# Kernel tuning notes

Measured on AMD Instinct MI355X. Metric: run time of the kernel, lower is better.

Reference implementation:

```python
import jax, jax.numpy as jnp
import numpy as np

B, S, D, H, DK, DV = 4, 4096, 512, 8, 64, 64
BUCKET = 64
NB = S // BUCKET  # number of hash buckets = 64


def layernorm(x, g, b, eps=1e-5):
    m = x.mean(-1, keepdims=True)
    v = ((x - m) ** 2).mean(-1, keepdims=True)
    return (x - m) * jax.lax.rsqrt(v + eps) * g + b


def lsh_attention(x_q, x_kv, Wq, Wk, Wv, Wo, g, b, rot, bucket_size):
    # x_q, x_kv: [B, S, D]; rot: [H, dk, NB//2] random LSH rotations
    Bq, Sq, _ = x_q.shape
    Hh, dk, _ = rot.shape
    q = jnp.einsum('bsd,dhk->bhsk', x_q, Wq)
    k = jnp.einsum('bsd,dhk->bhsk', x_kv, Wk)
    v = jnp.einsum('bsd,dhk->bhsk', x_kv, Wv)
    dv = v.shape[-1]

    def hash_buckets(t):
        r = jnp.einsum('bhsk,hkr->bhsr', t, rot)
        return jnp.argmax(jnp.concatenate([r, -r], axis=-1), axis=-1)  # [B,H,S]

    bq = hash_buckets(q)
    bk = hash_buckets(k)
    pos = jnp.arange(Sq)
    # stable sort by bucket (position breaks ties)
    perm_q = jnp.argsort(bq * Sq + pos, axis=-1)  # [B,H,S]
    perm_k = jnp.argsort(bk * Sq + pos, axis=-1)
    take = lambda t, p: jnp.take_along_axis(t, p[..., None], axis=2)
    nc = Sq // bucket_size
    cq = take(q, perm_q).reshape(Bq, Hh, nc, bucket_size, dk)
    ck = take(k, perm_k).reshape(Bq, Hh, nc, bucket_size, dk)
    cv = take(v, perm_k).reshape(Bq, Hh, nc, bucket_size, dv)
    bq_c = jnp.take_along_axis(bq, perm_q, axis=-1).reshape(Bq, Hh, nc, bucket_size)
    bk_c = jnp.take_along_axis(bk, perm_k, axis=-1).reshape(Bq, Hh, nc, bucket_size)
    # each query chunk attends to its own key chunk plus the previous one
    ckx = jnp.concatenate([jnp.roll(ck, 1, axis=2), ck], axis=3)
    cvx = jnp.concatenate([jnp.roll(cv, 1, axis=2), cv], axis=3)
    bkx = jnp.concatenate([jnp.roll(bk_c, 1, axis=2), bk_c], axis=3)
    scores = jnp.einsum('bhcid,bhcjd->bhcij', cq, ckx) * (dk ** -0.5)
    scores = jnp.where(bq_c[..., :, None] == bkx[..., None, :], scores, -1e9)
    attn = jax.nn.softmax(scores, axis=-1)
    o = jnp.einsum('bhcij,bhcjd->bhcid', attn, cvx).reshape(Bq, Hh, Sq, dv)
    o = take(o, jnp.argsort(perm_q, axis=-1))  # unsort
    o = o.transpose(0, 2, 1, 3).reshape(Bq, Sq, Hh * dv)
    return layernorm(x_q + o @ Wo, g, b)


def feed_forward(x, W1, b1, W2, b2, g, b):
    h = jax.nn.relu(x @ W1 + b1)
    return layernorm(x + h @ W2 + b2, g, b)


def setup_inputs() -> dict:
    key = jax.random.key(0)
    ks = jax.random.split(key, 16)
    f = jax.random.normal
    d = {
        'decoder_input': f(ks[0], (B, S, D), jnp.float32),
        'encoder_output': f(ks[1], (B, S, D), jnp.float32),
    }
    s = D ** -0.5
    for i, pfx in ((2, 'sa'), (7, 'ca')):
        d[pfx + '_Wq'] = f(ks[i], (D, H, DK)) * s
        d[pfx + '_Wk'] = f(ks[i + 1], (D, H, DK)) * s
        d[pfx + '_Wv'] = f(ks[i + 2], (D, H, DV)) * s
        d[pfx + '_Wo'] = f(ks[i + 3], (H * DV, D)) * s
        d[pfx + '_g'] = jnp.ones((D,), jnp.float32)
        d[pfx + '_b'] = jnp.zeros((D,), jnp.float32)
        d[pfx + '_rot'] = f(ks[i + 4], (H, DK, NB // 2))
    d['ff_W1'] = f(ks[12], (D, 4 * D)) * s
    d['ff_b1'] = jnp.zeros((4 * D,), jnp.float32)
    d['ff_W2'] = f(ks[13], (4 * D, D)) * ((4 * D) ** -0.5)
    d['ff_b2'] = jnp.zeros((D,), jnp.float32)
    d['ff_g'] = jnp.ones((D,), jnp.float32)
    d['ff_b'] = jnp.zeros((D,), jnp.float32)
    d['bucket_size'] = BUCKET
    return d


def reference(decoder_input, encoder_output, sa_Wq, sa_Wk, sa_Wv, sa_Wo, sa_g, sa_b, sa_rot, ca_Wq, ca_Wk, ca_Wv, ca_Wo, ca_g, ca_b, ca_rot, ff_W1, ff_b1, ff_W2, ff_b2, ff_g, ff_b, bucket_size):
    x = lsh_attention(decoder_input, decoder_input, sa_Wq, sa_Wk, sa_Wv, sa_Wo, sa_g, sa_b, sa_rot, bucket_size)
    x = lsh_attention(x, encoder_output, ca_Wq, ca_Wk, ca_Wv, ca_Wo, ca_g, ca_b, ca_rot, bucket_size)
    return feed_forward(x, ff_W1, ff_b1, ff_W2, ff_b2, ff_g, ff_b)
```

## Files before the change

### kernel.cpp

```cpp
#include <hip/hip_runtime.h>
#include <hip/hip_bf16.h>
#include <math.h>

typedef __hip_bfloat16 bf16;

#define B_ 4
#define S_ 4096
#define D_ 512
#define H_ 8
#define NC_ 64
#define M_ (B_*S_)
#define BH_ (B_*H_)

typedef __attribute__((ext_vector_type(8))) short bfrag;
typedef __attribute__((ext_vector_type(4))) float facc;

static __device__ __forceinline__ float tof(float x){ return x; }
static __device__ __forceinline__ float tof(bf16 x){ return __bfloat162float(x); }

static __device__ __forceinline__ float4 ld4g(const float* p) {
    return *reinterpret_cast<const float4*>(p);
}
static __device__ __forceinline__ float4 ld4g(const bf16* p) {
    short4 s = *reinterpret_cast<const short4*>(p);
    float4 r;
    r.x = __bfloat162float(*reinterpret_cast<const bf16*>(&s.x));
    r.y = __bfloat162float(*reinterpret_cast<const bf16*>(&s.y));
    r.z = __bfloat162float(*reinterpret_cast<const bf16*>(&s.z));
    r.w = __bfloat162float(*reinterpret_cast<const bf16*>(&s.w));
    return r;
}
static __device__ __forceinline__ void st4(float* p, float4 v) {
    *reinterpret_cast<float4*>(p) = v;
}
static __device__ __forceinline__ void st4(bf16* p, float4 v) {
    bf16 b0 = __float2bfloat16(v.x), b1 = __float2bfloat16(v.y);
    bf16 b2 = __float2bfloat16(v.z), b3 = __float2bfloat16(v.w);
    short4 s;
    s.x = *reinterpret_cast<short*>(&b0);
    s.y = *reinterpret_cast<short*>(&b1);
    s.z = *reinterpret_cast<short*>(&b2);
    s.w = *reinterpret_cast<short*>(&b3);
    *reinterpret_cast<short4*>(p) = s;
}

#define GLL(gp, lp) __builtin_amdgcn_global_load_lds( \
    (const __attribute__((address_space(1))) void*)(gp), \
    (__attribute__((address_space(3))) void*)(lp), 16, 0, 0)

template<int OUTMODE, int RES>
__global__ __launch_bounds__(256) void gemm_k(
    const float* __restrict__ A, const float* __restrict__ Bw,
    const float* __restrict__ res, float* __restrict__ out, int N, int K)
{
    const int BK = 32;
    __shared__ float At[32][132];
    __shared__ float Bs[32 * 128];

    int tid = threadIdx.x;
    int wave = tid >> 6;
    int nbx = N >> 7;
    int bx = blockIdx.x % nbx;
    int by = blockIdx.x / nbx;
    int row0 = by << 7;
    int col0 = bx << 7;
    int ty = tid >> 4;
    int tx = tid & 15;

    float acc[8][8];
    #pragma unroll
    for (int i = 0; i < 8; i++)
        #pragma unroll
        for (int j = 0; j < 8; j++) acc[i][j] = 0.f;

    for (int k0 = 0; k0 < K; k0 += BK) {
        #pragma unroll
        for (int c = 0; c < 4; c++) {
            int e = c * 256 + tid;
            GLL(Bw + (size_t)(k0 + (e >> 5)) * N + col0 + ((e & 31) << 2),
                &Bs[c * 1024 + (wave << 8)]);
        }
        #pragma unroll
        for (int c = 0; c < 4; c++) {
            int e = c * 256 + tid;
            int r = e >> 3, k4 = (e & 7) << 2;
            float4 t4 = ld4g(A + (size_t)(row0 + r) * K + k0 + k4);
            At[k4 + 0][r] = t4.x;
            At[k4 + 1][r] = t4.y;
            At[k4 + 2][r] = t4.z;
            At[k4 + 3][r] = t4.w;
        }
        __syncthreads();
        #pragma unroll
        for (int kk = 0; kk < BK; kk++) {
            float4 a0 = *reinterpret_cast<const float4*>(&At[kk][ty * 8]);
            float4 a1 = *reinterpret_cast<const float4*>(&At[kk][ty * 8 + 4]);
            float4 b0 = *reinterpret_cast<const float4*>(&Bs[kk * 128 + tx * 4]);
            float4 b1 = *reinterpret_cast<const float4*>(&Bs[kk * 128 + 64 + tx * 4]);
            float a[8] = {a0.x, a0.y, a0.z, a0.w, a1.x, a1.y, a1.z, a1.w};
            float bb[8] = {b0.x, b0.y, b0.z, b0.w, b1.x, b1.y, b1.z, b1.w};
            #pragma unroll
            for (int i = 0; i < 8; i++)
                #pragma unroll
                for (int j = 0; j < 8; j++) acc[i][j] += a[i] * bb[j];
        }
        __syncthreads();
    }

    #pragma unroll
    for (int i = 0; i < 8; i++) {
        int r = row0 + ty * 8 + i;
        #pragma unroll
        for (int j = 0; j < 8; j++) {
            int c = col0 + ((j >> 2) << 6) + tx * 4 + (j & 3);
            float v = acc[i][j];
            if (RES == 1) v += res[(size_t)r * N + c];
            if (OUTMODE == 0) {
                out[(size_t)r * N + c] = v;
            } else {
                int b = r >> 12, s = r & (S_ - 1);
                int h = c >> 6, kk2 = c & 63;
                out[((size_t)(b * H_ + h) * S_ + s) * 64 + kk2] = v;
            }
        }
    }
}

template<int OUTMODE, int RES, bool BIAS, bool RELU>
__global__ __launch_bounds__(256) void mgemm_k(
    const short* __restrict__ A, const short* __restrict__ Bt,
    const float* __restrict__ bias, const float* __restrict__ res,
    void* __restrict__ out, int N, int K)
{
    __shared__ short As[128 * 32];
    __shared__ short Bs[128 * 32];

    int tid = threadIdx.x;
    int wave = tid >> 6, lane = tid & 63;
    int nbx = N >> 7;
    int bx = blockIdx.x % nbx, by = blockIdx.x / nbx;
    int row0 = by << 7, col0 = bx << 7;
    int wr = wave >> 1, wc = wave & 1;
    int fr = lane & 15, fq = lane >> 4;

    facc acc[4][4];
    facc zero = {0.f, 0.f, 0.f, 0.f};
    #pragma unroll
    for (int m = 0; m < 4; m++)
        #pragma unroll
        for (int n = 0; n < 4; n++) acc[m][n] = zero;

    const short* gA = A + (size_t)(row0 + (wave << 5) + (lane >> 2)) * K + ((lane & 3) << 3);
    const short* gB = Bt + (size_t)(col0 + (wave << 5) + (lane >> 2)) * K + ((lane & 3) << 3);

    for (int k0 = 0; k0 < K; k0 += 32) {
        GLL(gA + k0,                 &As[wave << 10]);
        GLL(gA + k0 + (size_t)16 * K, &As[(wave << 10) + 512]);
        GLL(gB + k0,                 &Bs[wave << 10]);
        GLL(gB + k0 + (size_t)16 * K, &Bs[(wave << 10) + 512]);
        __syncthreads();

        bfrag av[4], bv[4];
        #pragma unroll
        for (int m = 0; m < 4; m++)
            av[m] = *reinterpret_cast<const bfrag*>(&As[(((wr << 6) + (m << 4) + fr) << 5) + (fq << 3)]);
        #pragma unroll
        for (int n = 0; n < 4; n++)
            bv[n] = *reinterpret_cast<const bfrag*>(&Bs[(((wc << 6) + (n << 4) + fr) << 5) + (fq << 3)]);
        #pragma unroll
        for (int m = 0; m < 4; m++)
            #pragma unroll
            for (int n = 0; n < 4; n++)
                acc[m][n] = __builtin_amdgcn_mfma_f32_16x16x32_bf16(av[m], bv[n], acc[m][n], 0, 0, 0);
        __syncthreads();
    }

    #pragma unroll
    for (int m = 0; m < 4; m++) {
        #pragma unroll
        for (int n = 0; n < 4; n++) {
            #pragma unroll
            for (int r = 0; r < 4; r++) {
                int row = row0 + (wr << 6) + (m << 4) + (fq << 2) + r;
                int col = col0 + (wc << 6) + (n << 4) + fr;
                float v = acc[m][n][r];
                if (BIAS) v += bias[col];
                if (RELU) v = fmaxf(v, 0.f);
                if (RES == 1) v += res[(size_t)row * N + col];
                if (OUTMODE == 0) {
                    ((float*)out)[(size_t)row * N + col] = v;
                } else if (OUTMODE == 1) {
                    ((bf16*)out)[(size_t)row * N + col] = __float2bfloat16(v);
                } else {
                    int b = row >> 12, s = row & (S_ - 1);
                    int h = col >> 6, kk2 = col & 63;
                    ((bf16*)out)[(((size_t)(b * H_ + h) * S_ + s) << 6) + kk2] = __float2bfloat16(v);
                }
            }
        }
    }
}

__global__ __launch_bounds__(256) void convw_k(
    const float* __restrict__ W, bf16* __restrict__ Wt, int N, int K)
{
    int i = blockIdx.x * 256 + threadIdx.x;
    int n = i / K, k = i % K;
    Wt[i] = __float2bfloat16(W[(size_t)k * N + n]);
}

__global__ __launch_bounds__(256) void wrot_k(
    const float* __restrict__ W, const float* __restrict__ rot,
    float* __restrict__ wrot)
{
    int d = blockIdx.x, t = threadIdx.x;
    int h = t >> 5, j = t & 31;
    float a = 0.f;
    #pragma unroll
    for (int k = 0; k < 64; k++)
        a += W[(size_t)(d * H_ + h) * 64 + k] * rot[(size_t)(h * 64 + k) * 32 + j];
    wrot[(size_t)d * 256 + t] = a;
}

__global__ __launch_bounds__(256) void cast_k(
    const float* __restrict__ x, bf16* __restrict__ y)
{
    size_t i = ((size_t)blockIdx.x * 256 + threadIdx.x) * 4;
    float4 v = *reinterpret_cast<const float4*>(x + i);
    y[i]     = __float2bfloat16(v.x);
    y[i + 1] = __float2bfloat16(v.y);
    y[i + 2] = __float2bfloat16(v.z);
    y[i + 3] = __float2bfloat16(v.w);
}

__global__ __launch_bounds__(256) void hash_k(
    const float* __restrict__ t, const float* __restrict__ rot,
    int* __restrict__ bucket)
{
    int bh = blockIdx.x >> 4;
    int st = blockIdx.x & 15;
    int h = bh % H_;
    __shared__ float rs[64][32];
    int tid = threadIdx.x;
    for (int e = tid; e < 2048; e += 256)
        rs[e >> 5][e & 31] = rot[h * 2048 + e];
    __syncthreads();

    int s = st * 256 + tid;
    const float* qr = t + ((size_t)bh * S_ + s) * 64;
    float qv[64];
    #pragma unroll
    for (int i = 0; i < 64; i++) qv[i] = qr[i];
    float r[32];
    #pragma unroll
    for (int j = 0; j < 32; j++) {
        float a = 0.f;
        #pragma unroll
        for (int kk = 0; kk < 64; kk++) a += qv[kk] * rs[kk][j];
        r[j] = a;
    }
    float best = -INFINITY; int bi = 0;
    #pragma unroll
    for (int j = 0; j < 32; j++) { if (r[j] > best) { best = r[j]; bi = j; } }
    #pragma unroll
    for (int j = 0; j < 32; j++) { float v = -r[j]; if (v > best) { best = v; bi = 32 + j; } }
    bucket[(size_t)bh * S_ + s] = bi;
}

__global__ __launch_bounds__(256) void amax_k(
    const float* __restrict__ r, int* __restrict__ bucket)
{
    int idx = blockIdx.x * 256 + threadIdx.x;
    int row = idx >> 3, h = idx & 7;
    const float* rr = r + (size_t)row * 256 + h * 32;
    float best = -INFINITY; int bi = 0;
    #pragma unroll
    for (int j = 0; j < 32; j++) { float v = rr[j]; if (v > best) { best = v; bi = j; } }
    #pragma unroll
    for (int j = 0; j < 32; j++) { float v = -rr[j]; if (v > best) { best = v; bi = 32 + j; } }
    int b = row >> 12, s = row & (S_ - 1);
    bucket[((size_t)(b * H_ + h)) * S_ + s] = bi;
}

__global__ __launch_bounds__(256) void sort_k(
    const int* __restrict__ bucket, int* __restrict__ perm)
{
    int bh = blockIdx.x;
    __shared__ int lb[S_];
    __shared__ int cnt[64 * 128];
    __shared__ int wtot[4];
    int tid = threadIdx.x;

    for (int i = tid; i < S_; i += 256) lb[i] = bucket[(size_t)bh * S_ + i];
    for (int i = tid; i < 8192; i += 256) cnt[i] = 0;
    __syncthreads();

    if (tid < 128) {
        int s0 = tid << 5;
        #pragma unroll
        for (int i = 0; i < 32; i++)
            cnt[(lb[s0 + i] << 7) + tid]++;
    }
    __syncthreads();

    int base = tid << 5;
    int tsum = 0;
    #pragma unroll
    for (int i = 0; i < 32; i++) tsum += cnt[base + i];
    int incl = tsum;
    #pragma unroll
    for (int off = 1; off < 64; off <<= 1) {
        int n = __shfl_up(incl, off, 64);
        if ((tid & 63) >= off) incl += n;
    }
    if ((tid & 63) == 63) wtot[tid >> 6] = incl;
    __syncthreads();
    int wbase = 0;
    for (int w = 0; w < (tid >> 6); w++) wbase += wtot[w];
    int run = wbase + incl - tsum;
    #pragma unroll
    for (int i = 0; i < 32; i++) {
        int c = cnt[base + i];
        cnt[base + i] = run;
        run += c;
    }
    __syncthreads();

    if (tid < 128) {
        int s0 = tid << 5;
        int* pr = perm + (size_t)bh * S_;
        #pragma unroll
        for (int i = 0; i < 32; i++) {
            int b = lb[s0 + i];
            int pos = cnt[(b << 7) + tid]++;
            pr[pos] = s0 + i;
        }
    }
}

template<typename T, typename OT>
__global__ __launch_bounds__(256, 4) void attn_k(
    const T* __restrict__ q, const T* __restrict__ k,
    const T* __restrict__ v, const int* __restrict__ bq,
    const int* __restrict__ bk, const int* __restrict__ permq,
    const int* __restrict__ permk, OT* __restrict__ o)
{
    int c = blockIdx.x % NC_;
    int bh = blockIdx.x / NC_;
    int b = bh / H_, h = bh % H_;
    __shared__ float kv[128][64];
    __shared__ int skx[128];
    __shared__ int bkx[128];
    int tid = threadIdx.x;
    const int qq = tid >> 2, u = tid & 3;
    const size_t bhS = (size_t)bh * S_;

    if (tid < 128) {
        int sidx = (tid < 64) ? (((c + NC_ - 1) & (NC_ - 1)) * 64 + tid)
                              : (c * 64 + (tid - 64));
        int sk = permk[bhS + sidx];
        skx[tid] = sk;
        bkx[tid] = bk[bhS + sk];
    }
    __syncthreads();

    {
        int rr = tid >> 4, c4 = (tid & 15) << 2;
        #pragma unroll
        for (int pass = 0; pass < 8; pass++) {
            int row = pass * 16 + rr;
            *reinterpret_cast<float4*>(&kv[row][c4]) =
                ld4g(k + (bhS + skx[row]) * 64 + c4);
        }
    }

    int sq = permq[bhS + c * 64 + qq];
    float4 qv[4];
    {
        const T* qr = q + (bhS + sq) * 64 + u * 16;
        #pragma unroll
        for (int i = 0; i < 4; i++) qv[i] = ld4g(qr + i * 4);
    }
    int bqi = bq[bhS + sq];
    __syncthreads();

    float p[32];
    #pragma unroll
    for (int g = 0; g < 4; g++) {
        float part[32];
        #pragma unroll
        for (int t = 0; t < 32; t++) {
            const float4* kr = reinterpret_cast<const float4*>(&kv[g * 32 + t][u << 4]);
            float4 k0 = kr[0], k1 = kr[1], k2 = kr[2], k3 = kr[3];
            float s0 = qv[0].x * k0.x + qv[0].y * k0.y + qv[0].z * k0.z + qv[0].w * k0.w;
            float s1 = qv[1].x * k1.x + qv[1].y * k1.y + qv[1].z * k1.z + qv[1].w * k1.w;
            float s2 = qv[2].x * k2.x + qv[2].y * k2.y + qv[2].z * k2.z + qv[2].w * k2.w;
            float s3 = qv[3].x * k3.x + qv[3].y * k3.y + qv[3].z * k3.z + qv[3].w * k3.w;
            part[t] = (s0 + s1) + (s2 + s3);
        }
        float keep[16];
        #pragma unroll
        for (int t = 0; t < 16; t++) {
            float lo = __shfl_xor(part[t], 2, 64);
            float hi = __shfl_xor(part[16 + t], 2, 64);
            keep[t] = (u < 2) ? part[t] + lo : part[16 + t] + hi;
        }
        #pragma unroll
        for (int t = 0; t < 8; t++) {
            float lo = __shfl_xor(keep[t], 1, 64);
            float hi = __shfl_xor(keep[8 + t], 1, 64);
            float s = ((u & 1) == 0) ? keep[t] + lo : keep[8 + t] + hi;
            int j = g * 32 + (u >> 1) * 16 + (u & 1) * 8 + t;
            p[g * 8 + t] = (bqi == bkx[j]) ? s * 0.125f : -1e9f;
        }
    }

    float m = -INFINITY;
    #pragma unroll
    for (int i = 0; i < 32; i++) m = fmaxf(m, p[i]);
    m = fmaxf(m, __shfl_xor(m, 1, 64));
    m = fmaxf(m, __shfl_xor(m, 2, 64));
    float l = 0.f;
    #pragma unroll
    for (int i = 0; i < 32; i++) { p[i] = __expf(p[i] - m); l += p[i]; }
    l += __shfl_xor(l, 1, 64);
    l += __shfl_xor(l, 2, 64);

    __syncthreads();
    {
        int rr = tid >> 4, c4 = (tid & 15) << 2;
        #pragma unroll
        for (int pass = 0; pass < 8; pass++) {
            int row = pass * 16 + rr;
            *reinterpret_cast<float4*>(&kv[row][c4]) =
                ld4g(v + (bhS + skx[row]) * 64 + c4);
        }
    }
    __syncthreads();

    float4 acc0 = make_float4(0.f, 0.f, 0.f, 0.f);
    float4 acc1 = make_float4(0.f, 0.f, 0.f, 0.f);
    float4 acc2 = make_float4(0.f, 0.f, 0.f, 0.f);
    float4 acc3 = make_float4(0.f, 0.f, 0.f, 0.f);
    int base = tid & ~3;
    #pragma unroll
    for (int j = 0; j < 128; j++) {
        const int uo = ((j >> 3) & 1) | (((j >> 4) & 1) << 1);
        const int slot = ((j >> 5) << 3) | (j & 7);
        float pj = __shfl(p[slot], base + uo, 64);
        const float4* vr = reinterpret_cast<const float4*>(&kv[j][u << 4]);
        float4 v0 = vr[0], v1 = vr[1], v2 = vr[2], v3 = vr[3];
        acc0.x += pj * v0.x; acc0.y += pj * v0.y; acc0.z += pj * v0.z; acc0.w += pj * v0.w;
        acc1.x += pj * v1.x; acc1.y += pj * v1.y; acc1.z += pj * v1.z; acc1.w += pj * v1.w;
        acc2.x += pj * v2.x; acc2.y += pj * v2.y; acc2.z += pj * v2.z; acc2.w += pj * v2.w;
        acc3.x += pj * v3.x; acc3.y += pj * v3.y; acc3.z += pj * v3.z; acc3.w += pj * v3.w;
    }
    float inv = 1.0f / l;
    OT* orow = o + ((size_t)b * S_ + sq) * 512 + h * 64 + (u << 4);
    st4(orow + 0,  make_float4(acc0.x * inv, acc0.y * inv, acc0.z * inv, acc0.w * inv));
    st4(orow + 4,  make_float4(acc1.x * inv, acc1.y * inv, acc1.z * inv, acc1.w * inv));
    st4(orow + 8,  make_float4(acc2.x * inv, acc2.y * inv, acc2.z * inv, acc2.w * inv));
    st4(orow + 12, make_float4(acc3.x * inv, acc3.y * inv, acc3.z * inv, acc3.w * inv));
}

template<bool BFC>
__global__ __launch_bounds__(256) void ln_k(
    const float* __restrict__ x, const float* __restrict__ g,
    const float* __restrict__ bvec, float* __restrict__ out,
    bf16* __restrict__ bfout)
{
    int row = blockIdx.x;
    int tid = threadIdx.x;
    __shared__ float red[256];
    const float* xr = x + (size_t)row * D_;
    float v0 = xr[tid], v1 = xr[tid + 256];
    red[tid] = v0 + v1;
    __syncthreads();
    for (int off = 128; off > 0; off >>= 1) {
        if (tid < off) red[tid] += red[tid + off];
        __syncthreads();
    }
    float mean = red[0] / 512.f;
    __syncthreads();
    float d0 = v0 - mean, d1 = v1 - mean;
    red[tid] = d0 * d0 + d1 * d1;
    __syncthreads();
    for (int off = 128; off > 0; off >>= 1) {
        if (tid < off) red[tid] += red[tid + off];
        __syncthreads();
    }
    float var = red[0] / 512.f;
    float rs = 1.0f / sqrtf(var + 1e-5f);
    float y0 = d0 * rs * g[tid] + bvec[tid];
    float y1 = d1 * rs * g[tid + 256] + bvec[tid + 256];
    out[(size_t)row * D_ + tid] = y0;
    out[(size_t)row * D_ + tid + 256] = y1;
    if (BFC) {
        bfout[(size_t)row * D_ + tid] = __float2bfloat16(y0);
        bfout[(size_t)row * D_ + tid + 256] = __float2bfloat16(y1);
    }
}

extern "C" void kernel_launch(void* const* d_in, const int* in_sizes, int n_in,
                              void* d_out, int out_size, void* d_ws, size_t ws_size,
                              hipStream_t stream)
{
    (void)in_sizes; (void)n_in; (void)out_size; (void)ws_size;
    const float* dec   = (const float*)d_in[0];
    const float* enc   = (const float*)d_in[1];
    const float* sa_Wq = (const float*)d_in[2];
    const float* sa_Wk = (const float*)d_in[3];
    const float* sa_Wv = (const float*)d_in[4];
    const float* sa_Wo = (const float*)d_in[5];
    const float* sa_g  = (const float*)d_in[6];
    const float* sa_b  = (const float*)d_in[7];
    const float* sa_rot= (const float*)d_in[8];
    const float* ca_Wq = (const float*)d_in[9];
    const float* ca_Wk = (const float*)d_in[10];
    const float* ca_Wv = (const float*)d_in[11];
    const float* ca_Wo = (const float*)d_in[12];
    const float* ca_g  = (const float*)d_in[13];
    const float* ca_b  = (const float*)d_in[14];
    const float* ca_rot= (const float*)d_in[15];
    const float* ff_W1 = (const float*)d_in[16];
    const float* ff_b1 = (const float*)d_in[17];
    const float* ff_W2 = (const float*)d_in[18];
    const float* ff_b2 = (const float*)d_in[19];
    const float* ff_g  = (const float*)d_in[20];
    const float* ff_b  = (const float*)d_in[21];

    char* ws = (char*)d_ws;
    const size_t MB = 1ull << 20;
    float* qb     = (float*)(ws + 0);
    float* kb     = (float*)(ws + 32*MB);
    float* vb     = (float*)(ws + 64*MB);
    float* ob     = (float*)(ws + 96*MB);
    float* act0   = (float*)(ws + 128*MB);
    bf16*  act0bf = (bf16*)(ws + 160*MB);
    float* rq     = (float*)(ws + 0);
    float* rk     = (float*)(ws + 17*MB);
    bf16*  cq     = (bf16*)(ws + 0);
    bf16*  ck     = (bf16*)(ws + 16*MB);
    bf16*  cv     = (bf16*)(ws + 32*MB);
    bf16*  caOut  = (bf16*)(ws + 48*MB);
    bf16*  encbf  = (bf16*)(ws + 64*MB);
    bf16*  act1bf = (bf16*)(ws + 80*MB);
    float* act1   = (float*)(ws + 96*MB);
    bf16*  hid    = (bf16*)(ws + 0);
    float* ffout  = (float*)(ws + 128*MB);
    bf16*  caWqt  = (bf16*)(ws + 176*MB);
    bf16*  caWkt  = (bf16*)(ws + 176*MB + 512*1024);
    bf16*  caWvt  = (bf16*)(ws + 177*MB);
    bf16*  caWot  = (bf16*)(ws + 177*MB + 512*1024);
    bf16*  ffW1t  = (bf16*)(ws + 178*MB);
    bf16*  ffW2t  = (bf16*)(ws + 180*MB);
    float* wrotq  = (float*)(ws + 182*MB);
    float* wrotk  = (float*)(ws + 182*MB + 512*1024);
    int*   bqb    = (int*)(ws + 183*MB);
    int*   bkb    = (int*)(ws + 183*MB + 512*1024);
    int*   pqb    = (int*)(ws + 184*MB);
    int*   pkb    = (int*)(ws + 184*MB + 512*1024);

    dim3 blk(256);
    const int g512  = (M_ / 128) * (512 / 128);
    const int g256  = (M_ / 128) * (256 / 128);
    const int g2048 = (M_ / 128) * (2048 / 128);

    wrot_k<<<512, blk, 0, stream>>>(ca_Wq, ca_rot, wrotq);
    wrot_k<<<512, blk, 0, stream>>>(ca_Wk, ca_rot, wrotk);
    convw_k<<<1024, blk, 0, stream>>>(ca_Wq, caWqt, 512, 512);
    convw_k<<<1024, blk, 0, stream>>>(ca_Wk, caWkt, 512, 512);
    convw_k<<<1024, blk, 0, stream>>>(ca_Wv, caWvt, 512, 512);
    convw_k<<<1024, blk, 0, stream>>>(ca_Wo, caWot, 512, 512);
    convw_k<<<4096, blk, 0, stream>>>(ff_W1, ffW1t, 2048, 512);
    convw_k<<<4096, blk, 0, stream>>>(ff_W2, ffW2t, 512, 2048);

    gemm_k<1,0><<<g512, blk, 0, stream>>>(dec, sa_Wq, nullptr, qb, 512, 512);
    gemm_k<1,0><<<g512, blk, 0, stream>>>(dec, sa_Wk, nullptr, kb, 512, 512);
    gemm_k<1,0><<<g512, blk, 0, stream>>>(dec, sa_Wv, nullptr, vb, 512, 512);
    hash_k<<<BH_ * 16, blk, 0, stream>>>(qb, sa_rot, bqb);
    hash_k<<<BH_ * 16, blk, 0, stream>>>(kb, sa_rot, bkb);
    sort_k<<<BH_, blk, 0, stream>>>(bqb, pqb);
    sort_k<<<BH_, blk, 0, stream>>>(bkb, pkb);
    attn_k<float,float><<<BH_ * NC_, blk, 0, stream>>>(qb, kb, vb, bqb, bkb, pqb, pkb, ob);
    gemm_k<0,1><<<g512, blk, 0, stream>>>(ob, sa_Wo, dec, act0, 512, 512);
    ln_k<true><<<M_, blk, 0, stream>>>(act0, sa_g, sa_b, act0, act0bf);

    gemm_k<0,0><<<g256, blk, 0, stream>>>(act0, wrotq, nullptr, rq, 256, 512);
    gemm_k<0,0><<<g256, blk, 0, stream>>>(enc,  wrotk, nullptr, rk, 256, 512);
    amax_k<<<M_ * 8 / 256, blk, 0, stream>>>(rq, bqb);
    amax_k<<<M_ * 8 / 256, blk, 0, stream>>>(rk, bkb);
    sort_k<<<BH_, blk, 0, stream>>>(bqb, pqb);
    sort_k<<<BH_, blk, 0, stream>>>(bkb, pkb);
    cast_k<<<M_ * 512 / 1024, blk, 0, stream>>>(enc, encbf);
    mgemm_k<2,0,false,false><<<g512, blk, 0, stream>>>((const short*)act0bf, (const short*)caWqt, nullptr, nullptr, cq, 512, 512);
    mgemm_k<2,0,false,false><<<g512, blk, 0, stream>>>((const short*)encbf, (const short*)caWkt, nullptr, nullptr, ck, 512, 512);
    mgemm_k<2,0,false,false><<<g512, blk, 0, stream>>>((const short*)encbf, (const short*)caWvt, nullptr, nullptr, cv, 512, 512);
    attn_k<bf16,bf16><<<BH_ * NC_, blk, 0, stream>>>(cq, ck, cv, bqb, bkb, pqb, pkb, caOut);
    mgemm_k<0,1,false,false><<<g512, blk, 0, stream>>>((const short*)caOut, (const short*)caWot, nullptr, act0, act1, 512, 512);
    ln_k<true><<<M_, blk, 0, stream>>>(act1, ca_g, ca_b, act1, act1bf);

    mgemm_k<1,0,true,true><<<g2048, blk, 0, stream>>>((const short*)act1bf, (const short*)ffW1t, ff_b1, nullptr, hid, 2048, 512);
    mgemm_k<0,1,true,false><<<g512, blk, 0, stream>>>((const short*)hid, (const short*)ffW2t, ff_b2, act1, ffout, 512, 2048);
    ln_k<false><<<M_, blk, 0, stream>>>(ffout, ff_g, ff_b, (float*)d_out, nullptr);
}
```

Baseline: 1.159 ms.

## Use 512-thread fp32 GEMM blocks and prefetch V rows into registers in attention

The fp32 GEMM now runs 512 threads per 128x128 tile, so each thread holds an 8x4 accumulator instead of 8x8. The aim is lower register pressure and higher occupancy, and the epilogue now uses vectorized float4 residual loads and stores. The attention kernel issues its gathered V loads into registers before the score computation, so their latency overlaps the QK and softmax work instead of stalling after the barrier. The cost is 32 extra registers per thread in attention and changed LDS padding in the GEMM, with a possible change in bank-conflict behaviour.

```diff
diff --git a/kernel.cpp b/kernel.cpp
--- a/kernel.cpp
+++ b/kernel.cpp
@@ -49,12 +49,12 @@
     (__attribute__((address_space(3))) void*)(lp), 16, 0, 0)
 
 template<int OUTMODE, int RES>
-__global__ __launch_bounds__(256) void gemm_k(
+__global__ __launch_bounds__(512, 4) void gemm_k(
     const float* __restrict__ A, const float* __restrict__ Bw,
     const float* __restrict__ res, float* __restrict__ out, int N, int K)
 {
     const int BK = 32;
-    __shared__ float At[32][132];
+    __shared__ float At[32][133];
     __shared__ float Bs[32 * 128];
 
     int tid = threadIdx.x;
@@ -64,25 +64,25 @@
     int by = blockIdx.x / nbx;
     int row0 = by << 7;
     int col0 = bx << 7;
-    int ty = tid >> 4;
-    int tx = tid & 15;
-
-    float acc[8][8];
+    int ty = tid >> 5;
+    int tx = tid & 31;
+
+    float acc[8][4];
     #pragma unroll
     for (int i = 0; i < 8; i++)
         #pragma unroll
-        for (int j = 0; j < 8; j++) acc[i][j] = 0.f;
+        for (int j = 0; j < 4; j++) acc[i][j] = 0.f;
 
     for (int k0 = 0; k0 < K; k0 += BK) {
         #pragma unroll
-        for (int c = 0; c < 4; c++) {
-            int e = c * 256 + tid;
+        for (int c = 0; c < 2; c++) {
+            int e = c * 512 + tid;
             GLL(Bw + (size_t)(k0 + (e >> 5)) * N + col0 + ((e & 31) << 2),
-                &Bs[c * 1024 + (wave << 8)]);
-        }
-        #pragma unroll
-        for (int c = 0; c < 4; c++) {
-            int e = c * 256 + tid;
+                &Bs[c * 2048 + (wave << 8)]);
+        }
+        #pragma unroll
+        for (int c = 0; c < 2; c++) {
+            int e = c * 512 + tid;
             int r = e >> 3, k4 = (e & 7) << 2;
             float4 t4 = ld4g(A + (size_t)(row0 + r) * K + k0 + k4);
             At[k4 + 0][r] = t4.x;
@@ -96,32 +96,31 @@
             float4 a0 = *reinterpret_cast<const float4*>(&At[kk][ty * 8]);
             float4 a1 = *reinterpret_cast<const float4*>(&At[kk][ty * 8 + 4]);
             float4 b0 = *reinterpret_cast<const float4*>(&Bs[kk * 128 + tx * 4]);
-            float4 b1 = *reinterpret_cast<const float4*>(&Bs[kk * 128 + 64 + tx * 4]);
             float a[8] = {a0.x, a0.y, a0.z, a0.w, a1.x, a1.y, a1.z, a1.w};
-            float bb[8] = {b0.x, b0.y, b0.z, b0.w, b1.x, b1.y, b1.z, b1.w};
+            float bb[4] = {b0.x, b0.y, b0.z, b0.w};
             #pragma unroll
             for (int i = 0; i < 8; i++)
                 #pragma unroll
-                for (int j = 0; j < 8; j++) acc[i][j] += a[i] * bb[j];
+                for (int j = 0; j < 4; j++) acc[i][j] += a[i] * bb[j];
         }
         __syncthreads();
     }
 
+    int c0 = col0 + tx * 4;
     #pragma unroll
     for (int i = 0; i < 8; i++) {
         int r = row0 + ty * 8 + i;
-        #pragma unroll
-        for (int j = 0; j < 8; j++) {
-            int c = col0 + ((j >> 2) << 6) + tx * 4 + (j & 3);
-            float v = acc[i][j];
-            if (RES == 1) v += res[(size_t)r * N + c];
-            if (OUTMODE == 0) {
-                out[(size_t)r * N + c] = v;
-            } else {
-                int b = r >> 12, s = r & (S_ - 1);
-                int h = c >> 6, kk2 = c & 63;
-                out[((size_t)(b * H_ + h) * S_ + s) * 64 + kk2] = v;
-            }
+        float4 v = make_float4(acc[i][0], acc[i][1], acc[i][2], acc[i][3]);
+        if (RES == 1) {
+            float4 rv = ld4g(res + (size_t)r * N + c0);
+            v.x += rv.x; v.y += rv.y; v.z += rv.z; v.w += rv.w;
+        }
+        if (OUTMODE == 0) {
+            st4(out + (size_t)r * N + c0, v);
+        } else {
+            int b = r >> 12, s = r & (S_ - 1);
+            int h = c0 >> 6, kk2 = c0 & 63;
+            st4(out + ((size_t)(b * H_ + h) * S_ + s) * 64 + kk2, v);
         }
     }
 }
@@ -364,14 +363,12 @@
     }
     __syncthreads();
 
-    {
-        int rr = tid >> 4, c4 = (tid & 15) << 2;
-        #pragma unroll
-        for (int pass = 0; pass < 8; pass++) {
-            int row = pass * 16 + rr;
-            *reinterpret_cast<float4*>(&kv[row][c4]) =
-                ld4g(k + (bhS + skx[row]) * 64 + c4);
-        }
+    const int rr = tid >> 4, c4 = (tid & 15) << 2;
+    #pragma unroll
+    for (int pass = 0; pass < 8; pass++) {
+        int row = pass * 16 + rr;
+        *reinterpret_cast<float4*>(&kv[row][c4]) =
+            ld4g(k + (bhS + skx[row]) * 64 + c4);
     }
 
     int sq = permq[bhS + c * 64 + qq];
@@ -383,6 +380,11 @@
     }
     int bqi = bq[bhS + sq];
     __syncthreads();
+
+    float4 vpre[8];
+    #pragma unroll
+    for (int pass = 0; pass < 8; pass++)
+        vpre[pass] = ld4g(v + (bhS + skx[pass * 16 + rr]) * 64 + c4);
 
     float p[32];
     #pragma unroll
@@ -427,15 +429,9 @@
     l += __shfl_xor(l, 2, 64);
 
     __syncthreads();
-    {
-        int rr = tid >> 4, c4 = (tid & 15) << 2;
-        #pragma unroll
-        for (int pass = 0; pass < 8; pass++) {
-            int row = pass * 16 + rr;
-            *reinterpret_cast<float4*>(&kv[row][c4]) =
-                ld4g(v + (bhS + skx[row]) * 64 + c4);
-        }
-    }
+    #pragma unroll
+    for (int pass = 0; pass < 8; pass++)
+        *reinterpret_cast<float4*>(&kv[pass * 16 + rr][c4]) = vpre[pass];
     __syncthreads();
 
     float4 acc0 = make_float4(0.f, 0.f, 0.f, 0.f);
@@ -562,6 +558,7 @@
     int*   pkb    = (int*)(ws + 184*MB + 512*1024);
 
     dim3 blk(256);
+    dim3 blk512(512);
     const int g512  = (M_ / 128) * (512 / 128);
     const int g256  = (M_ / 128) * (256 / 128);
     const int g2048 = (M_ / 128) * (2048 / 128);
@@ -575,19 +572,19 @@
     convw_k<<<4096, blk, 0, stream>>>(ff_W1, ffW1t, 2048, 512);
     convw_k<<<4096, blk, 0, stream>>>(ff_W2, ffW2t, 512, 2048);
 
-    gemm_k<1,0><<<g512, blk, 0, stream>>>(dec, sa_Wq, nullptr, qb, 512, 512);
-    gemm_k<1,0><<<g512, blk, 0, stream>>>(dec, sa_Wk, nullptr, kb, 512, 512);
-    gemm_k<1,0><<<g512, blk, 0, stream>>>(dec, sa_Wv, nullptr, vb, 512, 512);
+    gemm_k<1,0><<<g512, blk512, 0, stream>>>(dec, sa_Wq, nullptr, qb, 512, 512);
+    gemm_k<1,0><<<g512, blk512, 0, stream>>>(dec, sa_Wk, nullptr, kb, 512, 512);
+    gemm_k<1,0><<<g512, blk512, 0, stream>>>(dec, sa_Wv, nullptr, vb, 512, 512);
     hash_k<<<BH_ * 16, blk, 0, stream>>>(qb, sa_rot, bqb);
     hash_k<<<BH_ * 16, blk, 0, stream>>>(kb, sa_rot, bkb);
     sort_k<<<BH_, blk, 0, stream>>>(bqb, pqb);
     sort_k<<<BH_, blk, 0, stream>>>(bkb, pkb);
     attn_k<float,float><<<BH_ * NC_, blk, 0, stream>>>(qb, kb, vb, bqb, bkb, pqb, pkb, ob);
-    gemm_k<0,1><<<g512, blk, 0, stream>>>(ob, sa_Wo, dec, act0, 512, 512);
+    gemm_k<0,1><<<g512, blk512, 0, stream>>>(ob, sa_Wo, dec, act0, 512, 512);
     ln_k<true><<<M_, blk, 0, stream>>>(act0, sa_g, sa_b, act0, act0bf);
 
-    gemm_k<0,0><<<g256, blk, 0, stream>>>(act0, wrotq, nullptr, rq, 256, 512);
-    gemm_k<0,0><<<g256, blk, 0, stream>>>(enc,  wrotk, nullptr, rk, 256, 512);
+    gemm_k<0,0><<<g256, blk512, 0, stream>>>(act0, wrotq, nullptr, rq, 256, 512);
+    gemm_k<0,0><<<g256, blk512, 0, stream>>>(enc,  wrotk, nullptr, rk, 256, 512);
     amax_k<<<M_ * 8 / 256, blk, 0, stream>>>(rq, bqb);
     amax_k<<<M_ * 8 / 256, blk, 0, stream>>>(rk, bkb);
     sort_k<<<BH_, blk, 0, stream>>>(bqb, pqb);
```

New measurement: 1.227 ms. 5.8% more time.
